# Kernel tuning notes

Measured on AMD Instinct MI355X. Metric: run time of the kernel, lower is better.

Reference implementation:

```python
import jax, jax.numpy as jnp
import numpy as np

KERNEL_LIST = (4, 8)
STRIDE = 4
EXT = 1
NUM_HEADS = 4
KEY_DIM = 32   # head_dim * attn_ratio = 64 * 0.5
HEAD_DIM = 64
SCALE = KEY_DIM ** -0.5


def _pool_matrix(inp, out):
    # torch adaptive_avg_pool2d: window i covers [floor(i*inp/out), ceil((i+1)*inp/out))
    P = np.zeros((out, inp), np.float32)
    for i in range(out):
        s0 = (i * inp) // out
        e0 = -((-(i + 1) * inp) // out)
        P[i, s0:e0] = 1.0 / (e0 - s0)
    return jnp.asarray(P)


def _dwconv3(x, w, b):
    # depthwise 3x3 conv, padding 1 (groups == channels)
    y = jax.lax.conv_general_dilated(
        x, w, window_strides=(1, 1), padding=((1, 1), (1, 1)),
        feature_group_count=x.shape[1],
        dimension_numbers=("NCHW", "OIHW", "NCHW"))
    return y + b[None, :, None, None]


def _attention(x, qkv_w, qkv_b, proj_w, proj_b, pe_w, pe_b):
    B, C, H, W = x.shape
    N = H * W
    qkv = jnp.einsum("oc,bchw->bohw", qkv_w, x) + qkv_b[None, :, None, None]
    qkv = qkv.reshape(B, NUM_HEADS, 2 * KEY_DIM + HEAD_DIM, N)
    q = qkv[:, :, :KEY_DIM]                # (B,h,kd,N)
    k = qkv[:, :, KEY_DIM:2 * KEY_DIM]     # (B,h,kd,N)
    v = qkv[:, :, 2 * KEY_DIM:]            # (B,h,hd,N)
    attn = jax.nn.softmax(jnp.einsum("bhkn,bhkm->bhnm", q, k) * SCALE, axis=-1)
    # v @ attn^T : out[d,n] = sum_m v[d,m] * attn[n,m]
    o = jnp.einsum("bhdm,bhnm->bhdn", v, attn).reshape(B, C, H, W)
    o = o + _dwconv3(v.reshape(B, C, H, W), pe_w, pe_b)
    return jnp.einsum("oc,bchw->bohw", proj_w, o) + proj_b[None, :, None, None]


def _extract(xp, Kp, s):
    # overlapping patches; layout (N, C, Lh, Kp, Lw, Kp); window order is (lh, lw)
    N, C, Hp, Wp = xp.shape
    Lh = (Hp - Kp) // s + 1
    Lw = (Wp - Kp) // s + 1
    hi = jnp.arange(Lh)[:, None] * s + jnp.arange(Kp)[None, :]  # (Lh, Kp)
    wi = jnp.arange(Lw)[:, None] * s + jnp.arange(Kp)[None, :]
    p = xp[:, :, hi, :]          # (N, C, Lh, Kp, Wp)
    p = p[:, :, :, :, wi]        # (N, C, Lh, Kp, Lw, Kp)
    return p, Lh, Lw


def setup_inputs() -> dict:
    key = jax.random.key(0)
    ks = jax.random.split(key, 9)
    C = 256
    w = 0.02
    return {
        "x": jax.random.normal(ks[0], (8, C, 64, 64), jnp.float32),
        "qkv_w": jax.random.normal(ks[1], (512, C), jnp.float32) * w,
        "qkv_b": jax.random.normal(ks[2], (512,), jnp.float32) * w,
        "proj_w": jax.random.normal(ks[3], (C, C), jnp.float32) * w,
        "proj_b": jax.random.normal(ks[4], (C,), jnp.float32) * w,
        "attn_pe_w": jax.random.normal(ks[5], (C, 1, 3, 3), jnp.float32) * w,
        "attn_pe_b": jax.random.normal(ks[6], (C,), jnp.float32) * w,
        "dp_pe_w": jax.random.normal(ks[7], (C, 1, 3, 3), jnp.float32) * w,
        "dp_pe_b": jax.random.normal(ks[8], (C,), jnp.float32) * w,
    }


def reference(x, qkv_w, qkv_b, proj_w, proj_b, attn_pe_w, attn_pe_b, dp_pe_w, dp_pe_b):
    N, C, H, W = x.shape
    xp = jnp.pad(x, ((0, 0), (0, 0), (EXT, EXT), (EXT, EXT)), mode="edge")  # replicate pad
    outs = [x]
    for K in KERNEL_LIST:
        Kp = K + 2 * EXT
        p, Lh, Lw = _extract(xp, Kp, STRIDE)
        P = _pool_matrix(Kp, K)
        # adaptive avg pool Kp->K on both spatial dims; windows ordered (lh, lw)
        pooled = jnp.einsum("pi,ncaibj,qj->nabcpq", P, p, P)
        pooled = pooled.reshape(N * Lh * Lw, C, K, K)
        y = _dwconv3(pooled, dp_pe_w, dp_pe_b) + pooled
        a = _attention(y, qkv_w, qkv_b, proj_w, proj_b, attn_pe_w, attn_pe_b)
        # torch does a raw .view(N, C*K*K, L) on the (N*L, C, K, K) buffer
        cols = a.reshape(N, C, K, K, Lh, Lw)
        cols_p = cols.transpose(0, 1, 2, 4, 3, 5)  # (N, C, K, Lh, K, Lw)
        hh = jnp.arange(Lh)[None, :] * STRIDE + jnp.arange(K)[:, None]  # (K, Lh)
        ww = jnp.arange(Lw)[None, :] * STRIDE + jnp.arange(K)[:, None]  # (K, Lw)
        folded = jnp.zeros((N, C, H, W), x.dtype).at[
            :, :, hh[:, :, None, None], ww[None, None, :, :]].add(cols_p)
        count = jnp.zeros((1, 1, H, W), x.dtype).at[
            :, :, hh[:, :, None, None], ww[None, None, :, :]].add(
            jnp.ones((1, 1, K, Lh, K, Lw), x.dtype))
        outs.append(folded / count)
    return sum(outs) / len(outs)
```

## Files before the change

kernel.cpp:

```cpp
#include <hip/hip_runtime.h>
#include <hip/hip_bf16.h>

typedef __bf16 bf16x8 __attribute__((ext_vector_type(8)));
typedef float  f32x4  __attribute__((ext_vector_type(4)));

#define DEV static __device__ __forceinline__

DEV float bf2f(ushort u) { unsigned x = ((unsigned)u) << 16; return __uint_as_float(x); }
DEV ushort f2bf(float f) {
    unsigned u = __float_as_uint(f);
    unsigned r = (u + 0x7FFFu + ((u >> 16) & 1u)) >> 16;
    return (ushort)r;
}

typedef __attribute__((address_space(1))) const unsigned int gu32;
typedef __attribute__((address_space(3))) unsigned int lu32;
DEV void gload16(const ushort* g, ushort* l) {
    __builtin_amdgcn_global_load_lds((gu32*)g, (lu32*)l, 16, 0, 0);
}

__global__ __launch_bounds__(256) void f2bf_kernel(
    const float* __restrict__ src, ushort* __restrict__ dst)
{
    int i = (blockIdx.x * 256 + threadIdx.x) * 4;
    float4 v = *(const float4*)(src + i);
    ushort4 o;
    o.x = f2bf(v.x); o.y = f2bf(v.y); o.z = f2bf(v.z); o.w = f2bf(v.w);
    *(ushort4*)(dst + i) = o;
}

__global__ __launch_bounds__(256) void pe_prep_kernel(
    const float* __restrict__ apw, ushort* __restrict__ wt)
{
    int i = blockIdx.x * 256 + threadIdx.x;
    if (i < 9 * 256) {
        int tap = i >> 8, c = i & 255;
        wt[i] = f2bf(apw[c * 9 + tap]);
    }
}

__global__ __launch_bounds__(256) void box_kernel(
    const float* __restrict__ x,
    ushort* __restrict__ B)
{
    int br = blockIdx.x % 65; int g = blockIdx.x / 65;
    const float* xg = x + (size_t)g * 256 * 4096;
    ushort* Bg = B + (size_t)g * 65 * 65 * 256;
    const int r0 = max(br - 1, 0) * 64;
    const int r1 = min(br, 63) * 64;
    __shared__ float s[128][65];
    const int wl = threadIdx.x & 63, cq = threadIdx.x >> 6;
    const int c2 = threadIdx.x & 127, bh = threadIdx.x >> 7;
    for (int half = 0; half < 2; ++half) {
#pragma unroll 4
        for (int it = 0; it < 32; ++it) {
            int cl_ = it * 4 + cq;
            const float* xp = xg + (size_t)(half * 128 + cl_) * 4096;
            s[cl_][wl] = xp[r0 + wl] + xp[r1 + wl];
        }
        __syncthreads();
        for (int bc = bh; bc < 65; bc += 2) {
            float v = 0.25f * (s[c2][max(bc - 1, 0)] + s[c2][min(bc, 63)]);
            Bg[((size_t)br * 65 + bc) * 256 + half * 128 + c2] = f2bf(v);
        }
        __syncthreads();
    }
}

template<int K, int L>
__global__ __launch_bounds__(256) void pool_kernel(
    const ushort* __restrict__ B,
    const float* __restrict__ w9,
    const float* __restrict__ bias,
    ushort* __restrict__ y)
{
    constexpr int HF = K / 2;
    const int pk = blockIdx.x;
    const int lw = pk % L; int t = pk / L; const int lh = t % L; const int g = t / L;
    const int c = threadIdx.x;
    const ushort* Bg = B + (size_t)g * 65 * 65 * 256 + c;
    float pool[K][K];
#pragma unroll
    for (int p = 0; p < K; ++p) {
        const int br = lh * 4 + p + (p >= HF ? 1 : 0);
#pragma unroll
        for (int q = 0; q < K; ++q) {
            const int bc = lw * 4 + q + (q >= HF ? 1 : 0);
            pool[p][q] = bf2f(Bg[((size_t)br * 65 + bc) * 256]);
        }
    }
    float wv[9];
#pragma unroll
    for (int i = 0; i < 9; ++i) wv[i] = w9[c * 9 + i];
    const float bv = bias[c];
    ushort* yp = y + (size_t)pk * (K * K) * 256 + c;
#pragma unroll
    for (int p = 0; p < K; ++p) {
#pragma unroll
        for (int q = 0; q < K; ++q) {
            float a = pool[p][q] + bv;
#pragma unroll
            for (int dp = -1; dp <= 1; ++dp) {
#pragma unroll
                for (int dq = -1; dq <= 1; ++dq) {
                    int pp = p + dp, qq = q + dq;
                    if (pp >= 0 && pp < K && qq >= 0 && qq < K)
                        a += wv[(dp + 1) * 3 + (dq + 1)] * pool[pp][qq];
                }
            }
            yp[(p * K + q) * 256] = f2bf(a);
        }
    }
}

template<int OC, int EPI, int K, int L, int RT>
__global__ __launch_bounds__(256) void gemm_kernel(
    const ushort* __restrict__ act,
    const ushort* __restrict__ w,
    const float* __restrict__ bias,
    ushort* __restrict__ out_bf)
{
    __shared__ __attribute__((aligned(16))) ushort As[128][32];
    __shared__ __attribute__((aligned(16))) ushort Ws[128][32];
    constexpr int NT = OC / 128;
    const int id  = blockIdx.x;
    const int xc  = id & 7;
    const int ctb = (id >> 3) % NT;
    const int tt  = id / (8 * NT);
    const int rowt = tt * 8 + xc;
    if (rowt >= RT) return;
    const int tid  = threadIdx.x;
    const int n0   = rowt * 128;
    const int ch0  = ctb * 128;
    const int wv   = tid >> 6, lane = tid & 63;
    const int l15  = lane & 15, quad = lane >> 4;
    const int wm   = wv >> 1, wn = wv & 1;

    const int qlog = (lane & 3) ^ ((lane >> 3) & 3);
    const size_t soff = (size_t)(lane >> 2) * 256 + (size_t)qlog * 8;
    const ushort* aS0 = act + ((size_t)n0 + wv * 32) * 256 + soff;
    const ushort* wS0 = w   + ((size_t)ch0 + wv * 32) * 256 + soff;
    const ushort* aS1 = aS0 + 16 * 256;
    const ushort* wS1 = wS0 + 16 * 256;
    ushort* aD0 = &As[wv * 32][0];
    ushort* wD0 = &Ws[wv * 32][0];
    ushort* aD1 = aD0 + 16 * 32;
    ushort* wD1 = wD0 + 16 * 32;

    const int rcol = (quad ^ ((l15 >> 1) & 3)) * 8;
    f32x4 acc[4][4] = {};
    for (int k0 = 0; k0 < 256; k0 += 32) {
        gload16(aS0 + k0, aD0);
        gload16(aS1 + k0, aD1);
        gload16(wS0 + k0, wD0);
        gload16(wS1 + k0, wD1);
        __syncthreads();
        bf16x8 af[4], bw[4];
#pragma unroll
        for (int t = 0; t < 4; ++t) {
            af[t] = *(const bf16x8*)&As[wm * 64 + t * 16 + l15][rcol];
            bw[t] = *(const bf16x8*)&Ws[wn * 64 + t * 16 + l15][rcol];
        }
#pragma unroll
        for (int mt = 0; mt < 4; ++mt)
#pragma unroll
            for (int nt = 0; nt < 4; ++nt)
                acc[mt][nt] = __builtin_amdgcn_mfma_f32_16x16x32_bf16(af[mt], bw[nt], acc[mt][nt], 0, 0, 0);
        __syncthreads();
    }

    float bv[4];
#pragma unroll
    for (int nt = 0; nt < 4; ++nt) bv[nt] = bias[ch0 + wn * 64 + nt * 16 + l15];
#pragma unroll
    for (int mt = 0; mt < 4; ++mt) {
#pragma unroll
        for (int r = 0; r < 4; ++r) {
            const int n = n0 + wm * 64 + mt * 16 + quad * 4 + r;
            if (EPI == 0) {
                ushort* dst = out_bf + (size_t)n * OC + ch0 + wn * 64;
#pragma unroll
                for (int nt = 0; nt < 4; ++nt)
                    dst[nt * 16 + l15] = f2bf(acc[mt][nt][r] + bv[nt]);
            } else {
                constexpr int K2 = K * K;
                constexpr int LL = L * L;
                const int b_g   = n >> (K == 8 ? 6 : 4);
                const int pq    = n & (K2 - 1);
                const int gl    = b_g / LL;
                const int b_loc = b_g - gl * LL;
                const size_t base = (size_t)gl * (256 * K2 * LL) + (size_t)b_loc * 256 * K2 + pq;
#pragma unroll
                for (int nt = 0; nt < 4; ++nt) {
                    const int ch = ch0 + wn * 64 + nt * 16 + l15;
                    out_bf[base + (size_t)ch * K2] = f2bf(acc[mt][nt][r] + bv[nt]);
                }
            }
        }
    }
}

__global__ __launch_bounds__(128) void attn8_mfma_kernel(
    const ushort* __restrict__ qkv,
    const ushort* __restrict__ wt,
    const float* __restrict__ pe_b,
    ushort* __restrict__ o_out)
{
    constexpr float SCALE = 0.17677669529663687f;
    __shared__ __attribute__((aligned(16))) ushort Pl[64][72];
    __shared__ __attribute__((aligned(16))) ushort Vt[64][72];
    __shared__ __attribute__((aligned(16))) ushort Vr[64][72];
    __shared__ __attribute__((aligned(16))) ushort wsh[9][64];
    __shared__ float bsh[64];
    const int tid  = threadIdx.x;
    const int lane = tid & 63;
    const int ww   = tid >> 6;
    const int b    = blockIdx.x >> 2;
    const int h    = blockIdx.x & 3;
    const int cbase = h * 64;
    const int l15  = lane & 15, quad = lane >> 4;
    const ushort* base = qkv + (size_t)b * 64 * 512 + h * 128;

    if (tid < 72) {
        int tap = tid / 8, cl8 = (tid & 7) * 8;
        *(uint4*)&wsh[tap][cl8] = *(const uint4*)&wt[tap * 256 + cbase + cl8];
    }
    if (tid < 64) bsh[tid] = pe_b[cbase + tid];

    {
        const int m = lane;
        const ushort* vsrc = base + (size_t)m * 512 + 64 + ww * 32;
        const int d0 = ww * 32;
#pragma unroll
        for (int t = 0; t < 4; ++t) {
            uint4 vv = *(const uint4*)(vsrc + t * 8);
            *(uint4*)&Vr[m][d0 + t * 8] = vv;
            unsigned u[4] = {vv.x, vv.y, vv.z, vv.w};
#pragma unroll
            for (int e = 0; e < 4; ++e) {
                Vt[d0 + t * 8 + e * 2][m]     = (ushort)(u[e] & 0xFFFF);
                Vt[d0 + t * 8 + e * 2 + 1][m] = (ushort)(u[e] >> 16);
            }
        }
    }

    bf16x8 fq[2];
#pragma unroll
    for (int s = 0; s < 2; ++s) {
        int n = (ww + 2 * s) * 16 + l15;
        fq[s] = *(const bf16x8*)(base + (size_t)n * 512 + quad * 8);
    }
    f32x4 S[2][4];
#pragma unroll
    for (int mt = 0; mt < 4; ++mt) {
        int m = mt * 16 + l15;
        bf16x8 fk = *(const bf16x8*)(base + (size_t)m * 512 + 32 + quad * 8);
#pragma unroll
        for (int s = 0; s < 2; ++s) {
            f32x4 z = {0.f, 0.f, 0.f, 0.f};
            S[s][mt] = __builtin_amdgcn_mfma_f32_16x16x32_bf16(fq[s], fk, z, 0, 0, 0);
        }
    }
    __syncthreads();

    {
        const int d8  = (tid & 7) * 8;
        const int nb  = tid >> 3;
        float pe[4][8];
#pragma unroll
        for (int e = 0; e < 8; ++e) {
            float pb = bsh[d8 + e];
#pragma unroll
            for (int it = 0; it < 4; ++it) pe[it][e] = pb;
        }
#pragma unroll
        for (int tap = 0; tap < 9; ++tap) {
            const int dp = tap / 3 - 1, dq = tap % 3 - 1;
            uint4 wv4 = *(const uint4*)&wsh[tap][d8];
            unsigned uw[4] = {wv4.x, wv4.y, wv4.z, wv4.w};
            float wlo[4], whi[4];
#pragma unroll
            for (int e2 = 0; e2 < 4; ++e2) {
                wlo[e2] = __uint_as_float(uw[e2] << 16);
                whi[e2] = __uint_as_float(uw[e2] & 0xFFFF0000u);
            }
#pragma unroll
            for (int it = 0; it < 4; ++it) {
                const int n = nb + 16 * it;
                const int pp = (n >> 3) + dp, qq = (n & 7) + dq;
                if (pp >= 0 && pp < 8 && qq >= 0 && qq < 8) {
                    uint4 vv = *(const uint4*)&Vr[pp * 8 + qq][d8];
                    unsigned uv[4] = {vv.x, vv.y, vv.z, vv.w};
#pragma unroll
                    for (int e2 = 0; e2 < 4; ++e2) {
                        float vlo = __uint_as_float(uv[e2] << 16);
                        float vhi = __uint_as_float(uv[e2] & 0xFFFF0000u);
                        pe[it][2 * e2]     += wlo[e2] * vlo;
                        pe[it][2 * e2 + 1] += whi[e2] * vhi;
                    }
                }
            }
        }
#pragma unroll
        for (int it = 0; it < 4; ++it) {
            const int n = nb + 16 * it;
            ushort pk[8];
#pragma unroll
            for (int e = 0; e < 8; ++e) pk[e] = f2bf(pe[it][e]);
            *(uint4*)&Pl[n][d8] = *(const uint4*)pk;
        }
    }
    __syncthreads();

    f32x4 O[2][4];
#pragma unroll
    for (int s = 0; s < 2; ++s)
#pragma unroll
        for (int dt = 0; dt < 4; ++dt)
#pragma unroll
            for (int r = 0; r < 4; ++r)
                O[s][dt][r] = bf2f(Pl[(ww + 2 * s) * 16 + quad * 4 + r][dt * 16 + l15]);

#pragma unroll
    for (int s = 0; s < 2; ++s) {
#pragma unroll
        for (int r = 0; r < 4; ++r) {
            float mx = -1e30f;
#pragma unroll
            for (int mt = 0; mt < 4; ++mt) { S[s][mt][r] *= SCALE; mx = fmaxf(mx, S[s][mt][r]); }
            mx = fmaxf(mx, __shfl_xor(mx, 1));
            mx = fmaxf(mx, __shfl_xor(mx, 2));
            mx = fmaxf(mx, __shfl_xor(mx, 4));
            mx = fmaxf(mx, __shfl_xor(mx, 8));
            float sum = 0.f;
#pragma unroll
            for (int mt = 0; mt < 4; ++mt) { float e = __expf(S[s][mt][r] - mx); S[s][mt][r] = e; sum += e; }
            sum += __shfl_xor(sum, 1);
            sum += __shfl_xor(sum, 2);
            sum += __shfl_xor(sum, 4);
            sum += __shfl_xor(sum, 8);
            float inv = 1.f / sum;
#pragma unroll
            for (int mt = 0; mt < 4; ++mt) S[s][mt][r] *= inv;
        }
    }
    __syncthreads();

#pragma unroll
    for (int s = 0; s < 2; ++s)
#pragma unroll
        for (int r = 0; r < 4; ++r) {
            int n = (ww + 2 * s) * 16 + quad * 4 + r;
#pragma unroll
            for (int mt = 0; mt < 4; ++mt)
                Pl[n][mt * 16 + l15] = f2bf(S[s][mt][r]);
        }
    __syncthreads();

#pragma unroll
    for (int ks = 0; ks < 2; ++ks) {
        bf16x8 fp[2], fv[4];
#pragma unroll
        for (int s = 0; s < 2; ++s)
            fp[s] = *(const bf16x8*)&Pl[(ww + 2 * s) * 16 + l15][ks * 32 + quad * 8];
#pragma unroll
        for (int dt = 0; dt < 4; ++dt)
            fv[dt] = *(const bf16x8*)&Vt[dt * 16 + l15][ks * 32 + quad * 8];
#pragma unroll
        for (int s = 0; s < 2; ++s)
#pragma unroll
            for (int dt = 0; dt < 4; ++dt)
                O[s][dt] = __builtin_amdgcn_mfma_f32_16x16x32_bf16(fp[s], fv[dt], O[s][dt], 0, 0, 0);
    }

#pragma unroll
    for (int s = 0; s < 2; ++s) {
#pragma unroll
        for (int r = 0; r < 4; ++r) {
            int n = (ww + 2 * s) * 16 + quad * 4 + r;
#pragma unroll
            for (int dt = 0; dt < 4; ++dt)
                Pl[n][dt * 16 + l15] = f2bf(O[s][dt][r]);
        }
    }
    __syncthreads();

#pragma unroll
    for (int it = 0; it < 4; ++it) {
        int cidx = it * 128 + tid;
        int row = cidx >> 3, c8 = (cidx & 7) * 8;
        uint4 v = *(const uint4*)&Pl[row][c8];
        *(uint4*)(o_out + (size_t)(b * 64 + row) * 256 + cbase + c8) = v;
    }
}

template<int K>
__global__ __launch_bounds__(256) void attn_kernel(
    const ushort* __restrict__ qkv,
    const ushort* __restrict__ wt,
    const float* __restrict__ pe_b,
    ushort* __restrict__ o_out)
{
    constexpr int NSP = K * K;
    constexpr float SCALE = 0.17677669529663687f;
    __shared__ float q_s[32][NSP];
    __shared__ float k_s[32][NSP];
    __shared__ float v_s[64][NSP + 1];
    __shared__ float S[NSP][NSP + 1];
    const int tid = threadIdx.x;
    const int h = blockIdx.x & 3;
    const int b = blockIdx.x >> 2;
    {
        int n0 = tid >> 4;
        int rr = (tid & 15) * 8;
        for (int nb = 0; nb < NSP; nb += 16) {
            int n = nb + n0;
            const ushort* src = qkv + (size_t)(b * NSP + n) * 512 + h * 128 + rr;
            uint4 pk = *(const uint4*)src;
            ushort us[8];
            *(uint4*)us = pk;
#pragma unroll
            for (int j = 0; j < 8; ++j) {
                int r = rr + j;
                float f = bf2f(us[j]);
                if (r < 32) q_s[r][n] = f * SCALE;
                else if (r < 64) k_s[r - 32][n] = f;
                else v_s[r - 64][n] = f;
            }
        }
    }
    __syncthreads();
    for (int idx = tid; idx < NSP * NSP; idx += 256) {
        int n = idx / NSP, m = idx % NSP;
        float a = 0.f;
#pragma unroll
        for (int d = 0; d < 32; ++d) a += q_s[d][n] * k_s[d][m];
        S[n][m] = a;
    }
    __syncthreads();
    for (int n = tid; n < NSP; n += 256) {
        float mx = -1e30f;
        for (int m = 0; m < NSP; ++m) mx = fmaxf(mx, S[n][m]);
        float sum = 0.f;
        for (int m = 0; m < NSP; ++m) { float e = __expf(S[n][m] - mx); S[n][m] = e; sum += e; }
        float inv = 1.f / sum;
        for (int m = 0; m < NSP; ++m) S[n][m] *= inv;
    }
    __syncthreads();
    for (int idx = tid; idx < 64 * NSP; idx += 256) {
        int d = idx & 63, n = idx >> 6;
        float a = 0.f;
        for (int m = 0; m < NSP; ++m) a += v_s[d][m] * S[n][m];
        int c = h * 64 + d;
        int p = n / K, q = n % K;
        float pe = pe_b[c];
#pragma unroll
        for (int dp = -1; dp <= 1; ++dp) {
#pragma unroll
            for (int dq = -1; dq <= 1; ++dq) {
                int pp = p + dp, qq = q + dq;
                if (pp >= 0 && pp < K && qq >= 0 && qq < K)
                    pe += bf2f(wt[((dp + 1) * 3 + (dq + 1)) * 256 + c]) * v_s[d][pp * K + qq];
            }
        }
        o_out[(size_t)(b * NSP + n) * 256 + c] = f2bf(a + pe);
    }
}

__global__ __launch_bounds__(256) void final_kernel(
    const float* __restrict__ x,
    const ushort* __restrict__ s8,
    const ushort* __restrict__ s4,
    float* __restrict__ out)
{
    const int c2 = blockIdx.x & 255;
    const int g  = blockIdx.x >> 8;
    const ushort* s8g = s8 + (size_t)g * (256 * 64 * 225);
    const ushort* s4g = s4 + (size_t)g * (256 * 16 * 256);
    const float third = 1.f / 3.f;
#pragma unroll 2
    for (int it = 0; it < 16; ++it) {
        int pix = it * 256 + threadIdx.x;
        int h = pix >> 6, w = pix & 63;
        int f4 = ((((c2 * 4 + (h & 3)) * 4 + (w & 3)) * 16 + (h >> 2)) * 16) + (w >> 2);
        float v4 = bf2f(s4g[f4]);
        int lh_lo = (h >= 8) ? ((h - 4) >> 2) : 0, lh_hi = min(14, h >> 2);
        int lw_lo = (w >= 8) ? ((w - 4) >> 2) : 0, lw_hi = min(14, w >> 2);
        float v8 = 0.f;
        for (int lh2 = lh_lo; lh2 <= lh_hi; ++lh2) {
            int p2 = h - lh2 * 4;
            for (int lw2 = lw_lo; lw2 <= lw_hi; ++lw2) {
                int q2 = w - lw2 * 4;
                int f8 = (((c2 * 8 + p2) * 8 + q2) * 15 + lh2) * 15 + lw2;
                v8 += bf2f(s8g[f8]);
            }
        }
        float inv = 1.f / (float)((lh_hi - lh_lo + 1) * (lw_hi - lw_lo + 1));
        size_t off = ((size_t)(g * 256 + c2)) * 4096 + pix;
        out[off] = (x[off] + v8 * inv + v4) * third;
    }
}

extern "C" void kernel_launch(void* const* d_in, const int* in_sizes, int n_in,
                              void* d_out, int out_size, void* d_ws, size_t ws_size,
                              hipStream_t stream)
{
    const float* x      = (const float*)d_in[0];
    const float* qkv_w  = (const float*)d_in[1];
    const float* qkv_b  = (const float*)d_in[2];
    const float* proj_w = (const float*)d_in[3];
    const float* proj_b = (const float*)d_in[4];
    const float* apw    = (const float*)d_in[5];
    const float* apb    = (const float*)d_in[6];
    const float* dpw    = (const float*)d_in[7];
    const float* dpb    = (const float*)d_in[8];
    float* out = (float*)d_out;

    const size_t S8_B = 8ull * 225 * 256 * 64 * 2;
    const size_t S4_B = 8ull * 256 * 256 * 16 * 2;
    const size_t Y_B  = 4ull * 14400 * 256 * 2;
    const size_t Q_B  = 4ull * 14400 * 512 * 2;
    const size_t W_B  = (512ull * 256 + 256ull * 256 + 9ull * 256) * 2;
    const size_t B_B  = 8ull * 65 * 65 * 256 * 2;
    if (ws_size < S8_B + S4_B + Y_B + Q_B + W_B + B_B) {
        hipMemsetAsync(d_out, 0x46, 4, stream);
        return;
    }
    ushort* s8    = (ushort*)d_ws;
    ushort* s4    = s8 + S8_B / 2;
    ushort* ybuf  = s4 + S4_B / 2;
    ushort* qbuf  = ybuf + Y_B / 2;
    ushort* qw_bf = qbuf + Q_B / 2;
    ushort* pw_bf = qw_bf + 512 * 256;
    ushort* wt    = pw_bf + 256 * 256;
    ushort* Bbuf  = (ushort*)((char*)d_ws + S8_B + S4_B + Y_B + Q_B + W_B);

    f2bf_kernel<<<128, 256, 0, stream>>>(qkv_w, qw_bf);
    f2bf_kernel<<<64, 256, 0, stream>>>(proj_w, pw_bf);
    pe_prep_kernel<<<9, 256, 0, stream>>>(apw, wt);
    box_kernel<<<8 * 65, 256, 0, stream>>>(x, Bbuf);

    for (int hf = 0; hf < 2; ++hf) {
        ushort* B_h = Bbuf + (size_t)hf * 4 * 65 * 65 * 256;
        ushort* s8_h = s8 + (size_t)hf * 4 * 225 * 256 * 64;
        pool_kernel<8, 15><<<4 * 225, 256, 0, stream>>>(B_h, dpw, dpb, ybuf);
        gemm_kernel<512, 0, 8, 15, 450><<<57 * 8 * 4, 256, 0, stream>>>(ybuf, qw_bf, qkv_b, qbuf);
        attn8_mfma_kernel<<<900 * 4, 128, 0, stream>>>(qbuf, wt, apb, ybuf);
        gemm_kernel<256, 1, 8, 15, 450><<<57 * 8 * 2, 256, 0, stream>>>(ybuf, pw_bf, proj_b, s8_h);
    }
    pool_kernel<4, 16><<<8 * 256, 256, 0, stream>>>(Bbuf, dpw, dpb, ybuf);
    gemm_kernel<512, 0, 4, 16, 256><<<32 * 8 * 4, 256, 0, stream>>>(ybuf, qw_bf, qkv_b, qbuf);
    attn_kernel<4><<<8 * 256 * 4, 256, 0, stream>>>(qbuf, wt, apb, ybuf);
    gemm_kernel<256, 1, 4, 16, 256><<<32 * 8 * 2, 256, 0, stream>>>(ybuf, pw_bf, proj_b, s4);

    final_kernel<<<2048, 256, 0, stream>>>(x, s8, s4, out);
}
```

Baseline: 411.0 us.

## Replace scalar K=4 attention kernel with per-wave MFMA attention kernel

The generic scalar-FP32 attention kernel for the 4x4 window is replaced by a dedicated kernel. Each block now handles one window and each wave one head, instead of one block per (window, head). QK^T and PV are computed with bf16 16x16x32 MFMA instructions, and softmax is done with in-register shuffles, removing the shared-memory S matrix and several block barriers. The depthwise positional-encoding conv is folded into the MFMA accumulator initialisation. This cuts the block count by four and uses matrix cores, at the cost of bf16 rounding of the probabilities and of the pe term before accumulation.

```diff
diff --git a/kernel.cpp b/kernel.cpp
--- a/kernel.cpp
+++ b/kernel.cpp
@@ -394,76 +394,156 @@
     }
 }
 
-template<int K>
-__global__ __launch_bounds__(256) void attn_kernel(
+__global__ __launch_bounds__(256) void attn4_mfma_kernel(
     const ushort* __restrict__ qkv,
     const ushort* __restrict__ wt,
     const float* __restrict__ pe_b,
     ushort* __restrict__ o_out)
 {
-    constexpr int NSP = K * K;
     constexpr float SCALE = 0.17677669529663687f;
-    __shared__ float q_s[32][NSP];
-    __shared__ float k_s[32][NSP];
-    __shared__ float v_s[64][NSP + 1];
-    __shared__ float S[NSP][NSP + 1];
-    const int tid = threadIdx.x;
-    const int h = blockIdx.x & 3;
-    const int b = blockIdx.x >> 2;
+    __shared__ __attribute__((aligned(16))) ushort wsh[9][256];
+    __shared__ float bsh[256];
+    __shared__ __attribute__((aligned(16))) ushort Vt4[4][64][32];
+    __shared__ __attribute__((aligned(16))) ushort VP[4][16][64];
+    __shared__ __attribute__((aligned(16))) ushort Pm[4][16][32];
+    const int tid  = threadIdx.x;
+    const int lane = tid & 63;
+    const int w    = tid >> 6;
+    const int b    = blockIdx.x;
+    const int h    = w;
+    const int cbase = h * 64;
+    const int l15  = lane & 15, quad = lane >> 4;
+    const ushort* base = qkv + (size_t)b * 16 * 512 + h * 128;
+
+    for (int i = tid; i < 9 * 32; i += 256) {
+        int tap = i >> 5, c8 = (i & 31) * 8;
+        *(uint4*)&wsh[tap][c8] = *(const uint4*)&wt[tap * 256 + c8];
+    }
+    bsh[tid] = pe_b[tid];
+    __syncthreads();
+
     {
-        int n0 = tid >> 4;
-        int rr = (tid & 15) * 8;
-        for (int nb = 0; nb < NSP; nb += 16) {
-            int n = nb + n0;
-            const ushort* src = qkv + (size_t)(b * NSP + n) * 512 + h * 128 + rr;
-            uint4 pk = *(const uint4*)src;
-            ushort us[8];
-            *(uint4*)us = pk;
-#pragma unroll
-            for (int j = 0; j < 8; ++j) {
-                int r = rr + j;
-                float f = bf2f(us[j]);
-                if (r < 32) q_s[r][n] = f * SCALE;
-                else if (r < 64) k_s[r - 32][n] = f;
-                else v_s[r - 64][n] = f;
+        uint4 z = {0u, 0u, 0u, 0u};
+#pragma unroll
+        for (int t = 0; t < 4; ++t)
+            *(uint4*)&Vt4[w][t * 16 + (lane >> 2)][(lane & 3) * 8] = z;
+        *(uint4*)&Pm[w][lane >> 2][(lane & 3) * 8] = z;
+    }
+
+    {
+        const int m = lane & 15, dblk = lane >> 4;
+        const ushort* vsrc = base + (size_t)m * 512 + 64 + dblk * 16;
+        uint4 v0 = *(const uint4*)(vsrc);
+        uint4 v1 = *(const uint4*)(vsrc + 8);
+        *(uint4*)&VP[w][m][dblk * 16]     = v0;
+        *(uint4*)&VP[w][m][dblk * 16 + 8] = v1;
+        ushort us[16];
+        *(uint4*)&us[0] = v0; *(uint4*)&us[8] = v1;
+        const int mb = m >> 3, m7 = m & 7;
+#pragma unroll
+        for (int e = 0; e < 16; ++e) {
+            int d = dblk * 16 + e;
+            Vt4[w][d][((mb ^ (d & 3)) << 3) + m7] = us[e];
+        }
+    }
+
+    bf16x8 fq = *(const bf16x8*)(base + (size_t)l15 * 512 + quad * 8);
+    bf16x8 fk = *(const bf16x8*)(base + (size_t)l15 * 512 + 32 + quad * 8);
+    f32x4 z4 = {0.f, 0.f, 0.f, 0.f};
+    f32x4 S = __builtin_amdgcn_mfma_f32_16x16x32_bf16(fq, fk, z4, 0, 0, 0);
+
+    float p[4];
+#pragma unroll
+    for (int r = 0; r < 4; ++r) {
+        float v = S[r] * SCALE;
+        float mx = v;
+        mx = fmaxf(mx, __shfl_xor(mx, 1));
+        mx = fmaxf(mx, __shfl_xor(mx, 2));
+        mx = fmaxf(mx, __shfl_xor(mx, 4));
+        mx = fmaxf(mx, __shfl_xor(mx, 8));
+        float e = __expf(v - mx);
+        float sum = e;
+        sum += __shfl_xor(sum, 1);
+        sum += __shfl_xor(sum, 2);
+        sum += __shfl_xor(sum, 4);
+        sum += __shfl_xor(sum, 8);
+        p[r] = e / sum;
+    }
+#pragma unroll
+    for (int r = 0; r < 4; ++r) {
+        int n = quad * 4 + r;
+        Pm[w][n][(((l15 >> 3) ^ (n & 3)) << 3) + (l15 & 7)] = f2bf(p[r]);
+    }
+
+    float pe[2][8];
+    const int n_ = lane & 15;
+    const int pp0 = n_ >> 2, qq0 = n_ & 3;
+#pragma unroll
+    for (int it = 0; it < 2; ++it) {
+        int ch = (lane >> 4) + it * 4;
+#pragma unroll
+        for (int e = 0; e < 8; ++e) pe[it][e] = bsh[cbase + ch * 8 + e];
+    }
+#pragma unroll
+    for (int tap = 0; tap < 9; ++tap) {
+        const int dp = tap / 3 - 1, dq = tap % 3 - 1;
+        const int pp = pp0 + dp, qq = qq0 + dq;
+        if (pp >= 0 && pp < 4 && qq >= 0 && qq < 4) {
+            const int mm = pp * 4 + qq;
+#pragma unroll
+            for (int it = 0; it < 2; ++it) {
+                int ch = (lane >> 4) + it * 4;
+                uint4 wv4 = *(const uint4*)&wsh[tap][cbase + ch * 8];
+                uint4 vv  = *(const uint4*)&VP[w][mm][ch * 8];
+                unsigned uw[4] = {wv4.x, wv4.y, wv4.z, wv4.w};
+                unsigned uv[4] = {vv.x, vv.y, vv.z, vv.w};
+#pragma unroll
+                for (int e2 = 0; e2 < 4; ++e2) {
+                    float wlo = __uint_as_float(uw[e2] << 16);
+                    float whi = __uint_as_float(uw[e2] & 0xFFFF0000u);
+                    float vlo = __uint_as_float(uv[e2] << 16);
+                    float vhi = __uint_as_float(uv[e2] & 0xFFFF0000u);
+                    pe[it][2 * e2]     += wlo * vlo;
+                    pe[it][2 * e2 + 1] += whi * vhi;
+                }
             }
         }
     }
-    __syncthreads();
-    for (int idx = tid; idx < NSP * NSP; idx += 256) {
-        int n = idx / NSP, m = idx % NSP;
-        float a = 0.f;
-#pragma unroll
-        for (int d = 0; d < 32; ++d) a += q_s[d][n] * k_s[d][m];
-        S[n][m] = a;
-    }
-    __syncthreads();
-    for (int n = tid; n < NSP; n += 256) {
-        float mx = -1e30f;
-        for (int m = 0; m < NSP; ++m) mx = fmaxf(mx, S[n][m]);
-        float sum = 0.f;
-        for (int m = 0; m < NSP; ++m) { float e = __expf(S[n][m] - mx); S[n][m] = e; sum += e; }
-        float inv = 1.f / sum;
-        for (int m = 0; m < NSP; ++m) S[n][m] *= inv;
-    }
-    __syncthreads();
-    for (int idx = tid; idx < 64 * NSP; idx += 256) {
-        int d = idx & 63, n = idx >> 6;
-        float a = 0.f;
-        for (int m = 0; m < NSP; ++m) a += v_s[d][m] * S[n][m];
-        int c = h * 64 + d;
-        int p = n / K, q = n % K;
-        float pe = pe_b[c];
-#pragma unroll
-        for (int dp = -1; dp <= 1; ++dp) {
-#pragma unroll
-            for (int dq = -1; dq <= 1; ++dq) {
-                int pp = p + dp, qq = q + dq;
-                if (pp >= 0 && pp < K && qq >= 0 && qq < K)
-                    pe += bf2f(wt[((dp + 1) * 3 + (dq + 1)) * 256 + c]) * v_s[d][pp * K + qq];
-            }
-        }
-        o_out[(size_t)(b * NSP + n) * 256 + c] = f2bf(a + pe);
+#pragma unroll
+    for (int it = 0; it < 2; ++it) {
+        int ch = (lane >> 4) + it * 4;
+        ushort pk[8];
+#pragma unroll
+        for (int e = 0; e < 8; ++e) pk[e] = f2bf(pe[it][e]);
+        *(uint4*)&VP[w][n_][ch * 8] = *(const uint4*)pk;
+    }
+
+    f32x4 O[4];
+#pragma unroll
+    for (int dt = 0; dt < 4; ++dt)
+#pragma unroll
+        for (int r = 0; r < 4; ++r)
+            O[dt][r] = bf2f(VP[w][quad * 4 + r][dt * 16 + l15]);
+
+    bf16x8 fp = *(const bf16x8*)&Pm[w][l15][((quad ^ (l15 & 3)) << 3)];
+#pragma unroll
+    for (int dt = 0; dt < 4; ++dt) {
+        bf16x8 fv = *(const bf16x8*)&Vt4[w][dt * 16 + l15][((quad ^ (l15 & 3)) << 3)];
+        O[dt] = __builtin_amdgcn_mfma_f32_16x16x32_bf16(fp, fv, O[dt], 0, 0, 0);
+    }
+
+#pragma unroll
+    for (int dt = 0; dt < 4; ++dt)
+#pragma unroll
+        for (int r = 0; r < 4; ++r)
+            VP[w][quad * 4 + r][dt * 16 + l15] = f2bf(O[dt][r]);
+
+#pragma unroll
+    for (int j = 0; j < 2; ++j) {
+        int idx = j * 64 + lane;
+        int row = idx >> 3, c8 = (idx & 7) * 8;
+        uint4 v = *(const uint4*)&VP[w][row][c8];
+        *(uint4*)(o_out + (size_t)(b * 16 + row) * 256 + cbase + c8) = v;
     }
 }
 
@@ -550,7 +630,7 @@
     }
     pool_kernel<4, 16><<<8 * 256, 256, 0, stream>>>(Bbuf, dpw, dpb, ybuf);
     gemm_kernel<512, 0, 4, 16, 256><<<32 * 8 * 4, 256, 0, stream>>>(ybuf, qw_bf, qkv_b, qbuf);
-    attn_kernel<4><<<8 * 256 * 4, 256, 0, stream>>>(qbuf, wt, apb, ybuf);
+    attn4_mfma_kernel<<<2048, 256, 0, stream>>>(qbuf, wt, apb, ybuf);
     gemm_kernel<256, 1, 4, 16, 256><<<32 * 8 * 2, 256, 0, stream>>>(ybuf, pw_bf, proj_b, s4);
 
     final_kernel<<<2048, 256, 0, stream>>>(x, s8, s4, out);
```

Result: faster. 383.8 us (-6.6%).
